# Kernel tuning notes

Hardware: AMD Instinct MI355X
Metric: run time of the kernel (lower is better)

Reference implementation:

```python
import jax, jax.numpy as jnp
import numpy as np

T = 0.07          # temperature (params[1])
B, N, D, C = 128, 100000, 128, 40  # batch, bank size (outputSize=K), feat dim (inputSize-1), n classes
STDV = 1.0 / np.sqrt((D + 1) / 3.0)  # init scale from __init__


def setup_inputs() -> dict:
    key = jax.random.key(0)
    k1, k2, k3, k4, k5, k6 = jax.random.split(key, 6)
    x = jax.random.normal(k1, (B, D), dtype=jnp.float32)
    x = x / jnp.linalg.norm(x, axis=1, keepdims=True)  # unit-norm features (keeps exp(out/T) in range)
    y = jax.random.randint(k2, (B,), 0, N)
    labels = jax.random.randint(k3, (B,), 0, C)
    bank_labels = jax.random.randint(k4, (N,), 0, C).astype(jnp.float32)
    mem_feats = (jax.random.uniform(k5, (N, D), dtype=jnp.float32) * 2.0 - 1.0) * STDV
    da_feats = (jax.random.uniform(k6, (N, D), dtype=jnp.float32) * 2.0 - 1.0) * STDV
    memory = jnp.concatenate([bank_labels[:, None], mem_feats], axis=1)      # [N, 1+D], col 0 = label
    memory_da = jnp.concatenate([bank_labels[:, None], da_feats], axis=1)    # [N, 1+D], col 0 = label
    return {"x": x, "y": y, "labels": labels, "memory_da": memory_da, "memory": memory}


def reference(x, y, labels, memory_da, memory):
    # NCEFunction.forward: out[b,n] = exp(x[b] . memory_da[n,1:] / T), Z-normalized per row (Z<0 branch)
    n_out = memory_da.shape[0]
    feats = memory_da[:, 1:]                               # [N, D] gathered features
    out = jnp.exp(jnp.einsum('bd,nd->bn', x, feats) / T)   # [B, N] (torch bmm over repeated bank)
    Z1 = out.mean(axis=1, keepdims=True) * n_out           # per-row Z estimate
    out = out / Z1
    # idx: per-label torch.where loop -> expressed densely as a boolean match matrix [B, N]
    idx_mask = memory_da[None, :, 0] == labels[:, None].astype(memory_da.dtype)
    return out, idx_mask
```

## Files before the change

kernel.cpp:

```cpp
#include <hip/hip_runtime.h>
#include <hip/hip_bf16.h>

#define NB 128
#define NMEM 100000
#define ND 128
constexpr float T_INV = 1.0f / 0.07f;

constexpr int LROW = ND + 8;
constexpr int NTW = NMEM / 16;
constexpr int GRID = 512;
constexpr int NWAVES = GRID * 4;
constexpr int ZSTRIDE = 16;

typedef __attribute__((ext_vector_type(8))) __bf16 bf16x8;
typedef __attribute__((ext_vector_type(4))) float f32x4;
struct bf4 { __bf16 a, b, c, d; };

template<bool PASS2>
__global__ __launch_bounds__(256, 2) void nce_wave(
    const float* __restrict__ x,
    const int* __restrict__ labels,
    const float* __restrict__ mem_da,
    float* __restrict__ zbuf,
    float* __restrict__ out,
    float* __restrict__ maskout)
{
  __shared__ __bf16 xs[NB * LROW];
  __shared__ float aux[NB];
  __shared__ float zl[NB];

  const int tid = threadIdx.x;

  const float4* x4 = (const float4*)x;
  float4 xv[16];
  #pragma unroll
  for (int i = 0; i < 16; ++i) xv[i] = x4[tid + i * 256];
  #pragma unroll
  for (int i = 0; i < 16; ++i) {
    int g4 = tid + i * 256;
    *(bf4*)&xs[(g4 >> 5) * LROW + (g4 & 31) * 4] =
        bf4{(__bf16)xv[i].x, (__bf16)xv[i].y, (__bf16)xv[i].z, (__bf16)xv[i].w};
  }
  if (tid < NB) {
    if (PASS2) aux[tid] = 1.0f / zbuf[tid * ZSTRIDE];
    else { aux[tid] = (float)labels[tid]; zl[tid] = 0.f; }
  }
  __syncthreads();

  const int wid = tid >> 6, lane = tid & 63, q = lane >> 4, l16 = lane & 15;
  const int wgid = blockIdx.x * 4 + wid;

  f32x4 am[8];
  #pragma unroll
  for (int mt = 0; mt < 8; ++mt) am[mt] = *(const f32x4*)&aux[mt * 16 + q * 4];

  f32x4 zacc[8];
  #pragma unroll
  for (int mt = 0; mt < 8; ++mt) zacc[mt] = (f32x4){0.f, 0.f, 0.f, 0.f};

  for (int t = wgid; t < NTW; t += NWAVES) {
    const float* rowp = mem_da + (size_t)(t * 16 + l16) * 129;
    float ln;
    if (!PASS2) ln = rowp[0];
    float bf[4][8];
    #pragma unroll
    for (int kc = 0; kc < 4; ++kc)
      __builtin_memcpy(&bf[kc][0], rowp + 1 + kc * 32 + q * 8, 32);
    bf16x8 bb[4];
    #pragma unroll
    for (int kc = 0; kc < 4; ++kc)
      #pragma unroll
      for (int j = 0; j < 8; ++j) bb[kc][j] = (__bf16)bf[kc][j];

    f32x4 acc[8];
    #pragma unroll
    for (int mt = 0; mt < 8; ++mt) acc[mt] = (f32x4){0.f, 0.f, 0.f, 0.f};
    #pragma unroll
    for (int kc = 0; kc < 4; ++kc) {
      const int ko = kc * 32 + q * 8;
      #pragma unroll
      for (int mt = 0; mt < 8; ++mt) {
        bf16x8 a = *(const bf16x8*)&xs[(mt * 16 + l16) * LROW + ko];
        acc[mt] = __builtin_amdgcn_mfma_f32_16x16x32_bf16(a, bb[kc], acc[mt], 0, 0, 0);
      }
    }

    const size_t n = (size_t)t * 16 + l16;
    #pragma unroll
    for (int mt = 0; mt < 8; ++mt) {
      #pragma unroll
      for (int r = 0; r < 4; ++r) {
        const size_t off = (size_t)(mt * 16 + q * 4 + r) * NMEM + n;
        if (!PASS2) {
          zacc[mt][r] += __expf(acc[mt][r] * T_INV);
          maskout[off] = (ln == am[mt][r]) ? 1.0f : 0.0f;
        } else {
          out[off] = __expf(acc[mt][r] * T_INV) * am[mt][r];
        }
      }
    }
  }

  if (!PASS2) {
    #pragma unroll
    for (int mt = 0; mt < 8; ++mt) {
      #pragma unroll
      for (int r = 0; r < 4; ++r) {
        float v = zacc[mt][r];
        v += __shfl_xor(v, 1);
        v += __shfl_xor(v, 2);
        v += __shfl_xor(v, 4);
        v += __shfl_xor(v, 8);
        if (l16 == 0) atomicAdd(&zl[mt * 16 + q * 4 + r], v);
      }
    }
    __syncthreads();
    if (tid < NB) atomicAdd(&zbuf[tid * ZSTRIDE], zl[tid]);
  }
}

extern "C" void kernel_launch(void* const* d_in, const int* in_sizes, int n_in,
                              void* d_out, int out_size, void* d_ws, size_t ws_size,
                              hipStream_t stream) {
  const float* x      = (const float*)d_in[0];
  const int* labels   = (const int*)d_in[2];
  const float* mem_da = (const float*)d_in[3];
  float* out     = (float*)d_out;
  float* maskout = out + (size_t)NB * NMEM;
  float* zbuf    = (float*)d_ws;

  hipMemsetAsync(zbuf, 0, NB * ZSTRIDE * sizeof(float), stream);
  nce_wave<false><<<GRID, 256, 0, stream>>>(x, labels, mem_da, zbuf, nullptr, maskout);
  nce_wave<true ><<<GRID, 256, 0, stream>>>(x, labels, mem_da, zbuf, out, nullptr);
}
```

Baseline: 207.7 us.

## Split mask into dedicated coalesced kernel and widen out-pass tiles to 64 columns

The first pass now only computes the per-row Z sums and copies the bank label column into workspace. A new kernel writes the mask with float4 coalesced stores from that compact label array, replacing the strided scalar stores that used to happen inside the MFMA loop. The output pass gives each wave a fixed 64-column block, with four 16-column subtiles, instead of grid-striding 16-column tiles. This aims for better store locality and more independent MFMA work per wave, at the cost of an extra launch and larger accumulator register use.

```diff
diff --git a/kernel.cpp b/kernel.cpp
--- a/kernel.cpp
+++ b/kernel.cpp
@@ -7,30 +7,30 @@
 constexpr float T_INV = 1.0f / 0.07f;
 
 constexpr int LROW = ND + 8;
+constexpr int ZSTRIDE = 16;
+
 constexpr int NTW = NMEM / 16;
-constexpr int GRID = 512;
-constexpr int NWAVES = GRID * 4;
-constexpr int ZSTRIDE = 16;
+constexpr int GRID_Z = 512;
+constexpr int NWAVES_Z = GRID_Z * 4;
+
+constexpr int NFULL = NMEM / 64;
+constexpr int GRID_O = 391;
 
 typedef __attribute__((ext_vector_type(8))) __bf16 bf16x8;
 typedef __attribute__((ext_vector_type(4))) float f32x4;
 struct bf4 { __bf16 a, b, c, d; };
 
-template<bool PASS2>
-__global__ __launch_bounds__(256, 2) void nce_wave(
+
+__global__ __launch_bounds__(256, 2) void nce_z(
     const float* __restrict__ x,
-    const int* __restrict__ labels,
     const float* __restrict__ mem_da,
     float* __restrict__ zbuf,
-    float* __restrict__ out,
-    float* __restrict__ maskout)
+    float* __restrict__ wslbl)
 {
   __shared__ __bf16 xs[NB * LROW];
-  __shared__ float aux[NB];
   __shared__ float zl[NB];
 
   const int tid = threadIdx.x;
-
   const float4* x4 = (const float4*)x;
   float4 xv[16];
   #pragma unroll
@@ -41,36 +41,29 @@
     *(bf4*)&xs[(g4 >> 5) * LROW + (g4 & 31) * 4] =
         bf4{(__bf16)xv[i].x, (__bf16)xv[i].y, (__bf16)xv[i].z, (__bf16)xv[i].w};
   }
-  if (tid < NB) {
-    if (PASS2) aux[tid] = 1.0f / zbuf[tid * ZSTRIDE];
-    else { aux[tid] = (float)labels[tid]; zl[tid] = 0.f; }
-  }
+  if (tid < NB) zl[tid] = 0.f;
   __syncthreads();
 
   const int wid = tid >> 6, lane = tid & 63, q = lane >> 4, l16 = lane & 15;
   const int wgid = blockIdx.x * 4 + wid;
 
-  f32x4 am[8];
-  #pragma unroll
-  for (int mt = 0; mt < 8; ++mt) am[mt] = *(const f32x4*)&aux[mt * 16 + q * 4];
-
   f32x4 zacc[8];
   #pragma unroll
   for (int mt = 0; mt < 8; ++mt) zacc[mt] = (f32x4){0.f, 0.f, 0.f, 0.f};
 
-  for (int t = wgid; t < NTW; t += NWAVES) {
+  for (int t = wgid; t < NTW; t += NWAVES_Z) {
     const float* rowp = mem_da + (size_t)(t * 16 + l16) * 129;
-    float ln;
-    if (!PASS2) ln = rowp[0];
-    float bf[4][8];
+    float ln = rowp[0];
+    if (q == 0) wslbl[t * 16 + l16] = ln;
+    float bfv[4][8];
     #pragma unroll
     for (int kc = 0; kc < 4; ++kc)
-      __builtin_memcpy(&bf[kc][0], rowp + 1 + kc * 32 + q * 8, 32);
+      __builtin_memcpy(&bfv[kc][0], rowp + 1 + kc * 32 + q * 8, 32);
     bf16x8 bb[4];
     #pragma unroll
     for (int kc = 0; kc < 4; ++kc)
       #pragma unroll
-      for (int j = 0; j < 8; ++j) bb[kc][j] = (__bf16)bf[kc][j];
+      for (int j = 0; j < 8; ++j) bb[kc][j] = (__bf16)bfv[kc][j];
 
     f32x4 acc[8];
     #pragma unroll
@@ -84,38 +77,118 @@
         acc[mt] = __builtin_amdgcn_mfma_f32_16x16x32_bf16(a, bb[kc], acc[mt], 0, 0, 0);
       }
     }
-
-    const size_t n = (size_t)t * 16 + l16;
-    #pragma unroll
-    for (int mt = 0; mt < 8; ++mt) {
-      #pragma unroll
-      for (int r = 0; r < 4; ++r) {
-        const size_t off = (size_t)(mt * 16 + q * 4 + r) * NMEM + n;
-        if (!PASS2) {
-          zacc[mt][r] += __expf(acc[mt][r] * T_INV);
-          maskout[off] = (ln == am[mt][r]) ? 1.0f : 0.0f;
-        } else {
-          out[off] = __expf(acc[mt][r] * T_INV) * am[mt][r];
+    #pragma unroll
+    for (int mt = 0; mt < 8; ++mt)
+      #pragma unroll
+      for (int r = 0; r < 4; ++r)
+        zacc[mt][r] += __expf(acc[mt][r] * T_INV);
+  }
+
+  #pragma unroll
+  for (int mt = 0; mt < 8; ++mt) {
+    #pragma unroll
+    for (int r = 0; r < 4; ++r) {
+      float v = zacc[mt][r];
+      v += __shfl_xor(v, 1);
+      v += __shfl_xor(v, 2);
+      v += __shfl_xor(v, 4);
+      v += __shfl_xor(v, 8);
+      if (l16 == 0) atomicAdd(&zl[mt * 16 + q * 4 + r], v);
+    }
+  }
+  __syncthreads();
+  if (tid < NB) atomicAdd(&zbuf[tid * ZSTRIDE], zl[tid]);
+}
+
+__global__ __launch_bounds__(256) void nce_mask(
+    const int* __restrict__ labels,
+    const float* __restrict__ wslbl,
+    float* __restrict__ maskout)
+{
+  const int m = blockIdx.x >> 1;
+  const int n0 = (blockIdx.x & 1) * (NMEM / 2);
+  const float lbl = (float)labels[m];
+  const float4* l4 = (const float4*)(wslbl + n0);
+  float4* o4 = (float4*)(maskout + (size_t)m * NMEM + n0);
+  for (int i = threadIdx.x; i < (NMEM / 2) / 4; i += 256) {
+    float4 v = l4[i];
+    o4[i] = make_float4(v.x == lbl ? 1.f : 0.f, v.y == lbl ? 1.f : 0.f,
+                        v.z == lbl ? 1.f : 0.f, v.w == lbl ? 1.f : 0.f);
+  }
+}
+
+__global__ __launch_bounds__(256, 2) void nce_out(
+    const float* __restrict__ x,
+    const float* __restrict__ mem_da,
+    const float* __restrict__ zbuf,
+    float* __restrict__ out)
+{
+  __shared__ __bf16 xs[NB * LROW];
+  __shared__ float aux[NB];
+
+  const int tid = threadIdx.x;
+  const float4* x4 = (const float4*)x;
+  float4 xv[16];
+  #pragma unroll
+  for (int i = 0; i < 16; ++i) xv[i] = x4[tid + i * 256];
+  #pragma unroll
+  for (int i = 0; i < 16; ++i) {
+    int g4 = tid + i * 256;
+    *(bf4*)&xs[(g4 >> 5) * LROW + (g4 & 31) * 4] =
+        bf4{(__bf16)xv[i].x, (__bf16)xv[i].y, (__bf16)xv[i].z, (__bf16)xv[i].w};
+  }
+  if (tid < NB) aux[tid] = 1.0f / zbuf[tid * ZSTRIDE];
+  __syncthreads();
+
+  const int wid = tid >> 6, lane = tid & 63, q = lane >> 4, l16 = lane & 15;
+  const int w = blockIdx.x * 4 + wid;
+  const int n0 = w * 64;
+  const int nsub = (w < NFULL) ? 4 : ((w == NFULL) ? 2 : 0);
+  if (nsub == 0) return;
+
+  f32x4 acc[4][8];
+  #pragma unroll
+  for (int s = 0; s < 4; ++s)
+    #pragma unroll
+    for (int mt = 0; mt < 8; ++mt) acc[s][mt] = (f32x4){0.f, 0.f, 0.f, 0.f};
+
+  #pragma unroll
+  for (int s = 0; s < 4; ++s) {
+    if (s < nsub) {
+      const float* rowp = mem_da + (size_t)(n0 + s * 16 + l16) * 129;
+      float bfv[4][8];
+      #pragma unroll
+      for (int kc = 0; kc < 4; ++kc)
+        __builtin_memcpy(&bfv[kc][0], rowp + 1 + kc * 32 + q * 8, 32);
+      bf16x8 bb[4];
+      #pragma unroll
+      for (int kc = 0; kc < 4; ++kc)
+        #pragma unroll
+        for (int j = 0; j < 8; ++j) bb[kc][j] = (__bf16)bfv[kc][j];
+      #pragma unroll
+      for (int kc = 0; kc < 4; ++kc) {
+        const int ko = kc * 32 + q * 8;
+        #pragma unroll
+        for (int mt = 0; mt < 8; ++mt) {
+          bf16x8 a = *(const bf16x8*)&xs[(mt * 16 + l16) * LROW + ko];
+          acc[s][mt] = __builtin_amdgcn_mfma_f32_16x16x32_bf16(a, bb[kc], acc[s][mt], 0, 0, 0);
         }
       }
     }
   }
 
-  if (!PASS2) {
-    #pragma unroll
-    for (int mt = 0; mt < 8; ++mt) {
-      #pragma unroll
-      for (int r = 0; r < 4; ++r) {
-        float v = zacc[mt][r];
-        v += __shfl_xor(v, 1);
-        v += __shfl_xor(v, 2);
-        v += __shfl_xor(v, 4);
-        v += __shfl_xor(v, 8);
-        if (l16 == 0) atomicAdd(&zl[mt * 16 + q * 4 + r], v);
-      }
-    }
-    __syncthreads();
-    if (tid < NB) atomicAdd(&zbuf[tid * ZSTRIDE], zl[tid]);
+  #pragma unroll
+  for (int mt = 0; mt < 8; ++mt) {
+    #pragma unroll
+    for (int r = 0; r < 4; ++r) {
+      const int m = mt * 16 + q * 4 + r;
+      const float rzm = aux[m];
+      const size_t base = (size_t)m * NMEM + n0 + l16;
+      #pragma unroll
+      for (int s = 0; s < 4; ++s)
+        if (s < nsub)
+          out[base + s * 16] = __expf(acc[s][mt][r] * T_INV) * rzm;
+    }
   }
 }
 
@@ -128,8 +201,10 @@
   float* out     = (float*)d_out;
   float* maskout = out + (size_t)NB * NMEM;
   float* zbuf    = (float*)d_ws;
+  float* wslbl   = (float*)((char*)d_ws + 8192);
 
   hipMemsetAsync(zbuf, 0, NB * ZSTRIDE * sizeof(float), stream);
-  nce_wave<false><<<GRID, 256, 0, stream>>>(x, labels, mem_da, zbuf, nullptr, maskout);
-  nce_wave<true ><<<GRID, 256, 0, stream>>>(x, labels, mem_da, zbuf, out, nullptr);
-}
+  nce_z   <<<GRID_Z, 256, 0, stream>>>(x, mem_da, zbuf, wslbl);
+  nce_mask<<<256,    256, 0, stream>>>(labels, wslbl, maskout);
+  nce_out <<<GRID_O, 256, 0, stream>>>(x, mem_da, zbuf, out);
+}
```

After: 214.2 us. +3.1%, slower.
